# Kernel optimization log

Hardware: AMD Instinct MI355X
Metric: run time of the kernel (lower is better)

## Reference

```python
import jax, jax.numpy as jnp
import numpy as np

J = 25
C_IN, HID, LAT = 3, 64, 32


def _graph_conv(x, A, W, b):
    # x: [N,T,J,Cin]; A: [J,J]; W: [Cin,Cout]; b: [Cout]
    A = jax.nn.softmax(A, axis=-1)
    # fused adjacency mix + projection: (A @ x) @ W + b
    x = jnp.einsum('ij,ntjc->ntic', A, x)
    return jnp.einsum('ntjc,cd->ntjd', x, W) + b


def setup_inputs() -> dict:
    key = jax.random.key(0)
    ks = jax.random.split(key, 13)
    x = jax.random.normal(ks[0], (32, 2048, J, C_IN), dtype=jnp.float32)
    eye = jnp.eye(J, dtype=jnp.float32)
    def lin(kw, kb, cin, cout):
        W = jax.random.normal(kw, (cin, cout), dtype=jnp.float32) / np.sqrt(cin)
        b = jax.random.normal(kb, (cout,), dtype=jnp.float32) * 0.01
        return W, b
    W1, b1 = lin(ks[1], ks[2], C_IN, HID)
    W2, b2 = lin(ks[3], ks[4], HID, LAT)
    W3, b3 = lin(ks[5], ks[6], LAT, HID)
    W4, b4 = lin(ks[7], ks[8], HID, C_IN)
    return {
        'x': x,
        'A1': eye, 'W1': W1, 'b1': b1,
        'A2': eye, 'W2': W2, 'b2': b2,
        'A3': eye, 'W3': W3, 'b3': b3,
        'A4': eye, 'W4': W4, 'b4': b4,
    }


def reference(x, A1, W1, b1, A2, W2, b2, A3, W3, b3, A4, W4, b4):
    h = jax.nn.relu(_graph_conv(x, A1, W1, b1))     # encoder_g1 + relu
    z = _graph_conv(h, A2, W2, b2)                  # encoder_g2 (no relu)
    h_dec = jax.nn.relu(_graph_conv(z, A3, W3, b3)) # decoder_g1 + relu
    out = _graph_conv(h_dec, A4, W4, b4)            # decoder_g2
    return out
```

## Files before the change

kernel.cpp:

```cpp
#include <hip/hip_runtime.h>
#include <math.h>

#define J 25
#define NJC 75
#define NWAVE 4
#define NTHREADS 256
#define NFPW 8
#define FRSZ 1056
#define SCRW (2 * FRSZ)

#define O_A1T  0
#define O_APP  1024
#define O_A4B  2048
#define O_W2T  3072
#define O_W3T  5120
#define O_W1T  7168
#define O_W4C  8192
#define O_B4   8512
#define O_BPPF 8576
#define CWS_SZ 8704

using bf16x2 = __attribute__((ext_vector_type(2))) __bf16;
using bf16x8 = __attribute__((ext_vector_type(8))) __bf16;
using f32x4  = __attribute__((ext_vector_type(4))) float;
using f32x16 = __attribute__((ext_vector_type(16))) float;

__device__ inline bf16x8 zero8() {
    bf16x8 z;
    #pragma unroll
    for (int j = 0; j < 8; j++) z[j] = (__bf16)0.f;
    return z;
}

#if defined(__has_builtin)
#if __has_builtin(__builtin_amdgcn_cvt_pk_bf16_f32)
#define HAVE_PK_BF16 1
#endif
#endif

__device__ inline bf16x2 cvt2(float a, float b) {
#ifdef HAVE_PK_BF16
    return __builtin_amdgcn_cvt_pk_bf16_f32(a, b);
#else
    bf16x2 r; r[0] = (__bf16)a; r[1] = (__bf16)b; return r;
#endif
}
__device__ inline bf16x8 pk8(const f32x16& acc, int st) {
    const int b = 8 * st;
    bf16x8 r;
    #pragma unroll
    for (int p = 0; p < 4; p++) {
        bf16x2 v = cvt2(acc[b + 2 * p], acc[b + 2 * p + 1]);
        r[2 * p] = v[0]; r[2 * p + 1] = v[1];
    }
    return r;
}

__global__ __launch_bounds__(NTHREADS, 3) void gcn_fused(
    const float* __restrict__ x,
    const float* __restrict__ A1, const float* __restrict__ W1, const float* __restrict__ b1,
    const float* __restrict__ A2, const float* __restrict__ W2, const float* __restrict__ b2,
    const float* __restrict__ A3, const float* __restrict__ W3, const float* __restrict__ b3,
    const float* __restrict__ A4, const float* __restrict__ W4, const float* __restrict__ b4,
    float* __restrict__ out)
{
    __shared__ __align__(16) __bf16 SCR[NWAVE * SCRW];
    __shared__ __align__(16) __bf16 CWS[CWS_SZ];

    const int t = threadIdx.x;

    {
        float* T   = (float*)SCR;
        float* bpp = T + 3125;
        float* T0 = T;        float* T1 = T + 625;  float* T2 = T + 1250;
        float* T3 = T + 1875; float* T4 = T + 2500;

        if (t < 100) {
            const int m = t / J, i = t % J;
            const float* Asrc = (m == 0) ? A1 : (m == 1) ? A2 : (m == 2) ? A3 : A4;
            float row[J];
            float mx = -1e30f;
            #pragma unroll
            for (int j = 0; j < J; j++) { row[j] = Asrc[i * J + j]; mx = fmaxf(mx, row[j]); }
            float s = 0.f;
            #pragma unroll
            for (int j = 0; j < J; j++) { row[j] = __expf(row[j] - mx); s += row[j]; }
            const float inv = 1.f / s;
            float* dst = T + m * 625 + i * J;
            #pragma unroll
            for (int j = 0; j < J; j++) dst[j] = row[j] * inv;
        }
        if (t < 64) {
            float s = b3[t];
            #pragma unroll
            for (int l = 0; l < 32; l++) s += W3[l * 64 + t] * b2[l];
            bpp[t] = s;
        }
        __syncthreads();

        for (int idx = t; idx < 625; idx += 256) {
            const int i = idx / J, jj = idx % J;
            float s = 0.f;
            #pragma unroll
            for (int k = 0; k < J; k++) s += T2[i * J + k] * T1[k * J + jj];
            T4[idx] = s;
        }
        __syncthreads();

        for (int i = t; i < 1024; i += 256) {
            const int b = i >> 8, n = (i >> 3) & 31, jj = i & 7;
            const int kn = 8 * b + jj;
            CWS[O_A1T + i] = (__bf16)((kn < J && n < J) ? T0[n * J + kn] : 0.f);
            const int s = b >> 1, h = b & 1, r = 8 * s + jj;
            const int k32 = (r & 3) + 8 * (r >> 2) + 4 * h;
            CWS[O_APP + i] = (__bf16)((k32 < J && n < J) ? T4[n * J + k32] : 0.f);
            CWS[O_A4B + i] = (__bf16)((k32 < J && n < J) ? T3[n * J + k32] : 0.f);
        }
        for (int i = t; i < 2048; i += 256) {
            {
                const int b = i >> 8, n = (i >> 3) & 31, jj = i & 7;
                const int s = b >> 1, h = b & 1, r = 8 * (s & 1) + jj;
                const int d = 32 * (s >> 1) + (r & 3) + 8 * (r >> 2) + 4 * h;
                CWS[O_W2T + i] = (__bf16)W2[d * 32 + n];
            }
            {
                const int tt = i >> 10, rr = i & 1023;
                const int b = rr >> 8, m = (rr >> 3) & 31, jj = rr & 7;
                const int s = b >> 1, h = b & 1, r = 8 * s + jj;
                const int l = (r & 3) + 8 * (r >> 2) + 4 * h;
                CWS[O_W3T + i] = (__bf16)W3[l * 64 + tt * 32 + m];
            }
        }
        for (int i = t; i < 1024; i += 256) {
            const int tt = i >> 9, rq = i & 511, hf = rq >> 8, q = rq & 255;
            const int m = q >> 3, c = q & 7, d = tt * 32 + m;
            float v = 0.f;
            if (hf == 0) {
                if (c < 3) v = W1[c * 64 + d];
                else if (c == 3) v = b1[d];
            }
            CWS[O_W1T + i] = (__bf16)v;
        }
        {
            const int c = t >> 6, b = (t >> 3) & 7, jj = t & 7;
            const int s = b >> 1, h = b & 1, r = 8 * (s & 1) + jj;
            const int d = 32 * (s >> 1) + (r & 3) + 8 * (r >> 2) + 4 * h;
            CWS[O_W4C + t] = (c < 3) ? (__bf16)W4[d * 3 + c] : (__bf16)0.f;
        }
        {
            float* fwB = (float*)(CWS + O_BPPF);
            if (t < 64) {
                const int g = t >> 4, h = (t >> 3) & 1, jj = t & 7;
                const int tt = g >> 1, st = g & 1;
                const int row32 = (jj & 3) + 16 * st + 8 * (jj >> 2) + 4 * h;
                fwB[t] = bpp[tt * 32 + row32];
            }
            float* fb4 = (float*)(CWS + O_B4);
            if (t >= 64 && t < 68) fb4[t - 64] = (t < 67) ? b4[t - 64] : 0.f;
        }
        __syncthreads();
    }

    const int w = t >> 6, lane = t & 63, ln = lane & 31, half = lane >> 5;
    const int fo = ln * 8;
    __bf16* scr = &SCR[w * SCRW];

    const long fbase = ((long)blockIdx.x * NWAVE + w) * NFPW;

    #pragma unroll
    for (int r = 0; r < 2; r++) {
        __bf16* s = scr + r * FRSZ;
        if (half == 0) s[(ln >> 3) * 264 + 24 + (ln & 7)] = (ln < J) ? (__bf16)1.f : (__bf16)0.f;
        if (lane < 21) s[3 * 264 + (lane / 7) * 8 + 1 + (lane % 7)] = (__bf16)0.f;
    }

    const int c0 = lane % 3, j0 = lane / 3;
    const int sx0 = (j0 >> 3) * 264 + c0 * 8 + (j0 & 7);
    const int i1 = 64 + lane, c1 = i1 % 3, j1 = i1 / 3;
    const int sx1 = (j1 >> 3) * 264 + c1 * 8 + (j1 & 7);

    {
        const long xb = fbase * NJC;
        float v0 = x[xb + lane];
        float v1 = (lane < NJC - 64) ? x[xb + 64 + lane] : 0.f;
        scr[sx0] = (__bf16)v0;
        if (lane < NJC - 64) scr[sx1] = (__bf16)v1;
    }
    float xv0 = 0.f, xv1 = 0.f;
    if (NFPW > 1) {
        const long xb = (fbase + 1) * NJC;
        xv0 = x[xb + lane];
        if (lane < NJC - 64) xv1 = x[xb + 64 + lane];
    }

    bf16x8 rA1T[2], rApp[2], rA4b[2], rW1[2], rW4[4];
    #pragma unroll
    for (int ks = 0; ks < 2; ks++) {
        rA1T[ks] = *(const bf16x8*)&CWS[O_A1T + (2 * ks + half) * 256 + fo];
        rApp[ks] = *(const bf16x8*)&CWS[O_APP + (2 * ks + half) * 256 + fo];
        rA4b[ks] = *(const bf16x8*)&CWS[O_A4B + (2 * ks + half) * 256 + fo];
        rW1[ks]  = *(const bf16x8*)&CWS[O_W1T + ks * 512 + half * 256 + fo];
    }
    #pragma unroll
    for (int ks = 0; ks < 4; ks++) {
        rW4[ks] = zero8();
        if (ln < 3) rW4[ks] = *(const bf16x8*)&CWS[O_W4C + ln * 64 + (half + 2 * ks) * 8];
    }
    f32x16 rB16[2];
    {
        const float* fwB = (const float*)(CWS + O_BPPF);
        #pragma unroll
        for (int tt = 0; tt < 2; tt++)
            #pragma unroll
            for (int st = 0; st < 2; st++) {
                f32x4 qa = *(const f32x4*)&fwB[32 * tt + 16 * st + 8 * half + 0];
                f32x4 qb = *(const f32x4*)&fwB[32 * tt + 16 * st + 8 * half + 4];
                #pragma unroll
                for (int j = 0; j < 4; j++) {
                    rB16[tt][8 * st + j]     = qa[j];
                    rB16[tt][8 * st + 4 + j] = qb[j];
                }
            }
    }
    float b4v = 0.f;
    if (ln < 3) b4v = ((const float*)(CWS + O_B4))[ln];

    f32x16 Z;
    #pragma unroll
    for (int z = 0; z < 16; z++) Z[z] = 0.f;

    for (int fi = 0; fi < NFPW; fi++) {
        const long f = fbase + fi;
        __bf16* sc = scr + (fi & 1) * FRSZ;

        if (fi + 1 < NFPW) {
            __bf16* sn = scr + ((fi + 1) & 1) * FRSZ;
            sn[sx0] = (__bf16)xv0;
            if (lane < NJC - 64) sn[sx1] = (__bf16)xv1;
        }
        if (fi + 2 < NFPW) {
            const long nxb = (f + 2) * NJC;
            xv0 = x[nxb + lane];
            if (lane < NJC - 64) xv1 = x[nxb + 64 + lane];
        }

        bf16x8 a0 = *(const bf16x8*)&sc[half * 264 + fo];
        bf16x8 a1 = *(const bf16x8*)&sc[(2 + half) * 264 + fo];
        f32x16 accY = __builtin_amdgcn_mfma_f32_32x32x16_bf16(a0, rA1T[0], Z, 0, 0, 0);
        accY = __builtin_amdgcn_mfma_f32_32x32x16_bf16(a1, rA1T[1], accY, 0, 0, 0);

        bf16x8 w2f[4];
        #pragma unroll
        for (int s = 0; s < 4; s++)
            w2f[s] = *(const bf16x8*)&CWS[O_W2T + (half + 2 * s) * 256 + fo];

        bf16x8 yb = zero8();
        if (half == 0) {
            bf16x2 q0 = cvt2(accY[0], accY[1]);
            bf16x2 q1 = cvt2(accY[2], accY[3]);
            yb[0] = q0[0]; yb[1] = q0[1]; yb[2] = q1[0]; yb[3] = q1[1];
        }
        bf16x8 hf[4];
        #pragma unroll
        for (int tt = 0; tt < 2; tt++) {
            f32x16 acc = __builtin_amdgcn_mfma_f32_32x32x16_bf16(rW1[tt], yb, Z, 0, 0, 0);
            #pragma unroll
            for (int z = 0; z < 16; z++) acc[z] = fmaxf(acc[z], 0.f);
            hf[2 * tt]     = pk8(acc, 0);
            hf[2 * tt + 1] = pk8(acc, 1);
        }

        f32x16 accU = __builtin_amdgcn_mfma_f32_32x32x16_bf16(hf[0], w2f[0], Z, 0, 0, 0);
        #pragma unroll
        for (int s = 1; s < 4; s++)
            accU = __builtin_amdgcn_mfma_f32_32x32x16_bf16(hf[s], w2f[s], accU, 0, 0, 0);
        bf16x8 uf[2] = { pk8(accU, 0), pk8(accU, 1) };

        bf16x8 w3f[4];
        #pragma unroll
        for (int tt = 0; tt < 2; tt++)
            #pragma unroll
            for (int ks = 0; ks < 2; ks++)
                w3f[tt * 2 + ks] = *(const bf16x8*)&CWS[O_W3T + tt * 1024 + (half + 2 * ks) * 256 + fo];

        f32x16 accV = __builtin_amdgcn_mfma_f32_32x32x16_bf16(uf[0], rApp[0], Z, 0, 0, 0);
        accV = __builtin_amdgcn_mfma_f32_32x32x16_bf16(uf[1], rApp[1], accV, 0, 0, 0);
        bf16x8 vf[2] = { pk8(accV, 0), pk8(accV, 1) };

        bf16x8 hd[4];
        #pragma unroll
        for (int tt = 0; tt < 2; tt++) {
            f32x16 acc = __builtin_amdgcn_mfma_f32_32x32x16_bf16(w3f[tt * 2 + 0], vf[0], rB16[tt], 0, 0, 0);
            acc = __builtin_amdgcn_mfma_f32_32x32x16_bf16(w3f[tt * 2 + 1], vf[1], acc, 0, 0, 0);
            #pragma unroll
            for (int z = 0; z < 16; z++) acc[z] = fmaxf(acc[z], 0.f);
            hd[2 * tt]     = pk8(acc, 0);
            hd[2 * tt + 1] = pk8(acc, 1);
        }

        f32x16 accP = __builtin_amdgcn_mfma_f32_32x32x16_bf16(hd[0], rW4[0], Z, 0, 0, 0);
        #pragma unroll
        for (int s = 1; s < 4; s++)
            accP = __builtin_amdgcn_mfma_f32_32x32x16_bf16(hd[s], rW4[s], accP, 0, 0, 0);
        bf16x8 pf[2] = { pk8(accP, 0), pk8(accP, 1) };

        f32x16 accO = __builtin_amdgcn_mfma_f32_32x32x16_bf16(rA4b[0], pf[0], Z, 0, 0, 0);
        accO = __builtin_amdgcn_mfma_f32_32x32x16_bf16(rA4b[1], pf[1], accO, 0, 0, 0);
        if (ln < 3) {
            const long ob = f * NJC;
            #pragma unroll
            for (int r = 0; r < 16; r++) {
                const int row = (r & 3) + 8 * (r >> 2) + 4 * half;
                if (row < J) out[ob + row * 3 + ln] = accO[r] + b4v;
            }
        }
    }
}

extern "C" void kernel_launch(void* const* d_in, const int* in_sizes, int n_in,
                              void* d_out, int out_size, void* d_ws, size_t ws_size,
                              hipStream_t stream)
{
    const float* x  = (const float*)d_in[0];
    const float* A1 = (const float*)d_in[1];
    const float* W1 = (const float*)d_in[2];
    const float* b1 = (const float*)d_in[3];
    const float* A2 = (const float*)d_in[4];
    const float* W2 = (const float*)d_in[5];
    const float* b2 = (const float*)d_in[6];
    const float* A3 = (const float*)d_in[7];
    const float* W3 = (const float*)d_in[8];
    const float* b3 = (const float*)d_in[9];
    const float* A4 = (const float*)d_in[10];
    const float* W4 = (const float*)d_in[11];
    const float* b4 = (const float*)d_in[12];
    float* out = (float*)d_out;
    (void)d_ws; (void)ws_size;

    const int NT = in_sizes[0] / NJC;
    const int nblocks = NT / (NWAVE * NFPW);

    gcn_fused<<<nblocks, NTHREADS, 0, stream>>>(
        x, A1, W1, b1, A2, W2, b2, A3, W3, b3, A4, W4, b4, out);
}
```

Measured before the change: 147.5 us.

## Hoist W2/W3 fragments to registers, transpose final MFMA, double frames per wave

Loads the W2 and W3 weight fragments from shared memory into registers once, instead of reloading them on every frame. The final MFMA's operands are swapped so the output comes out transposed: each lane stores its joint's three channels directly, replacing 16 predicated scattered stores. Frames per wave go from 8 to 16, the frame loop is fully unrolled, and pointer arithmetic is made incremental. Occupancy is lowered to 2 blocks per CU to leave room for the extra registers, which costs latency hiding and halves the grid size.

```diff
diff --git a/kernel.cpp b/kernel.cpp
--- a/kernel.cpp
+++ b/kernel.cpp
@@ -5,7 +5,7 @@
 #define NJC 75
 #define NWAVE 4
 #define NTHREADS 256
-#define NFPW 8
+#define NFPW 16
 #define FRSZ 1056
 #define SCRW (2 * FRSZ)
 
@@ -56,7 +56,7 @@
     return r;
 }
 
-__global__ __launch_bounds__(NTHREADS, 3) void gcn_fused(
+__global__ __launch_bounds__(NTHREADS, 2) void gcn_fused(
     const float* __restrict__ x,
     const float* __restrict__ A1, const float* __restrict__ W1, const float* __restrict__ b1,
     const float* __restrict__ A2, const float* __restrict__ W2, const float* __restrict__ b2,
@@ -167,6 +167,9 @@
 
     const long fbase = ((long)blockIdx.x * NWAVE + w) * NFPW;
 
+    const float* xp = x + fbase * NJC;
+    float* op = out + fbase * NJC;
+
     #pragma unroll
     for (int r = 0; r < 2; r++) {
         __bf16* s = scr + r * FRSZ;
@@ -178,22 +181,21 @@
     const int sx0 = (j0 >> 3) * 264 + c0 * 8 + (j0 & 7);
     const int i1 = 64 + lane, c1 = i1 % 3, j1 = i1 / 3;
     const int sx1 = (j1 >> 3) * 264 + c1 * 8 + (j1 & 7);
+    const bool ld2 = (lane < NJC - 64);
 
     {
-        const long xb = fbase * NJC;
-        float v0 = x[xb + lane];
-        float v1 = (lane < NJC - 64) ? x[xb + 64 + lane] : 0.f;
-        scr[sx0] = (__bf16)v0;
-        if (lane < NJC - 64) scr[sx1] = (__bf16)v1;
+        scr[sx0] = (__bf16)xp[lane];
+        if (ld2) scr[sx1] = (__bf16)xp[64 + lane];
+        xp += NJC;
     }
     float xv0 = 0.f, xv1 = 0.f;
     if (NFPW > 1) {
-        const long xb = (fbase + 1) * NJC;
-        xv0 = x[xb + lane];
-        if (lane < NJC - 64) xv1 = x[xb + 64 + lane];
-    }
-
-    bf16x8 rA1T[2], rApp[2], rA4b[2], rW1[2], rW4[4];
+        xv0 = xp[lane];
+        if (ld2) xv1 = xp[64 + lane];
+        xp += NJC;
+    }
+
+    bf16x8 rA1T[2], rApp[2], rA4b[2], rW1[2], rW2[4], rW3[4], rW4[4];
     #pragma unroll
     for (int ks = 0; ks < 2; ks++) {
         rA1T[ks] = *(const bf16x8*)&CWS[O_A1T + (2 * ks + half) * 256 + fo];
@@ -201,6 +203,14 @@
         rA4b[ks] = *(const bf16x8*)&CWS[O_A4B + (2 * ks + half) * 256 + fo];
         rW1[ks]  = *(const bf16x8*)&CWS[O_W1T + ks * 512 + half * 256 + fo];
     }
+    #pragma unroll
+    for (int ks = 0; ks < 4; ks++)
+        rW2[ks] = *(const bf16x8*)&CWS[O_W2T + (half + 2 * ks) * 256 + fo];
+    #pragma unroll
+    for (int tt = 0; tt < 2; tt++)
+        #pragma unroll
+        for (int ks = 0; ks < 2; ks++)
+            rW3[tt * 2 + ks] = *(const bf16x8*)&CWS[O_W3T + tt * 1024 + (half + 2 * ks) * 256 + fo];
     #pragma unroll
     for (int ks = 0; ks < 4; ks++) {
         rW4[ks] = zero8();
@@ -222,37 +232,34 @@
                 }
             }
     }
-    float b4v = 0.f;
-    if (ln < 3) b4v = ((const float*)(CWS + O_B4))[ln];
+    const float* fb4 = (const float*)(CWS + O_B4);
+    const float b40 = fb4[0], b41 = fb4[1], b42 = fb4[2];
 
     f32x16 Z;
     #pragma unroll
     for (int z = 0; z < 16; z++) Z[z] = 0.f;
 
+    const bool do_store = (lane < J);
+
+    #pragma unroll
     for (int fi = 0; fi < NFPW; fi++) {
-        const long f = fbase + fi;
         __bf16* sc = scr + (fi & 1) * FRSZ;
 
         if (fi + 1 < NFPW) {
             __bf16* sn = scr + ((fi + 1) & 1) * FRSZ;
             sn[sx0] = (__bf16)xv0;
-            if (lane < NJC - 64) sn[sx1] = (__bf16)xv1;
+            if (ld2) sn[sx1] = (__bf16)xv1;
         }
         if (fi + 2 < NFPW) {
-            const long nxb = (f + 2) * NJC;
-            xv0 = x[nxb + lane];
-            if (lane < NJC - 64) xv1 = x[nxb + 64 + lane];
+            xv0 = xp[lane];
+            if (ld2) xv1 = xp[64 + lane];
+            xp += NJC;
         }
 
         bf16x8 a0 = *(const bf16x8*)&sc[half * 264 + fo];
         bf16x8 a1 = *(const bf16x8*)&sc[(2 + half) * 264 + fo];
         f32x16 accY = __builtin_amdgcn_mfma_f32_32x32x16_bf16(a0, rA1T[0], Z, 0, 0, 0);
         accY = __builtin_amdgcn_mfma_f32_32x32x16_bf16(a1, rA1T[1], accY, 0, 0, 0);
-
-        bf16x8 w2f[4];
-        #pragma unroll
-        for (int s = 0; s < 4; s++)
-            w2f[s] = *(const bf16x8*)&CWS[O_W2T + (half + 2 * s) * 256 + fo];
 
         bf16x8 yb = zero8();
         if (half == 0) {
@@ -270,18 +277,11 @@
             hf[2 * tt + 1] = pk8(acc, 1);
         }
 
-        f32x16 accU = __builtin_amdgcn_mfma_f32_32x32x16_bf16(hf[0], w2f[0], Z, 0, 0, 0);
+        f32x16 accU = __builtin_amdgcn_mfma_f32_32x32x16_bf16(hf[0], rW2[0], Z, 0, 0, 0);
         #pragma unroll
         for (int s = 1; s < 4; s++)
-            accU = __builtin_amdgcn_mfma_f32_32x32x16_bf16(hf[s], w2f[s], accU, 0, 0, 0);
+            accU = __builtin_amdgcn_mfma_f32_32x32x16_bf16(hf[s], rW2[s], accU, 0, 0, 0);
         bf16x8 uf[2] = { pk8(accU, 0), pk8(accU, 1) };
-
-        bf16x8 w3f[4];
-        #pragma unroll
-        for (int tt = 0; tt < 2; tt++)
-            #pragma unroll
-            for (int ks = 0; ks < 2; ks++)
-                w3f[tt * 2 + ks] = *(const bf16x8*)&CWS[O_W3T + tt * 1024 + (half + 2 * ks) * 256 + fo];
 
         f32x16 accV = __builtin_amdgcn_mfma_f32_32x32x16_bf16(uf[0], rApp[0], Z, 0, 0, 0);
         accV = __builtin_amdgcn_mfma_f32_32x32x16_bf16(uf[1], rApp[1], accV, 0, 0, 0);
@@ -290,8 +290,8 @@
         bf16x8 hd[4];
         #pragma unroll
         for (int tt = 0; tt < 2; tt++) {
-            f32x16 acc = __builtin_amdgcn_mfma_f32_32x32x16_bf16(w3f[tt * 2 + 0], vf[0], rB16[tt], 0, 0, 0);
-            acc = __builtin_amdgcn_mfma_f32_32x32x16_bf16(w3f[tt * 2 + 1], vf[1], acc, 0, 0, 0);
+            f32x16 acc = __builtin_amdgcn_mfma_f32_32x32x16_bf16(rW3[tt * 2 + 0], vf[0], rB16[tt], 0, 0, 0);
+            acc = __builtin_amdgcn_mfma_f32_32x32x16_bf16(rW3[tt * 2 + 1], vf[1], acc, 0, 0, 0);
             #pragma unroll
             for (int z = 0; z < 16; z++) acc[z] = fmaxf(acc[z], 0.f);
             hd[2 * tt]     = pk8(acc, 0);
@@ -304,16 +304,14 @@
             accP = __builtin_amdgcn_mfma_f32_32x32x16_bf16(hd[s], rW4[s], accP, 0, 0, 0);
         bf16x8 pf[2] = { pk8(accP, 0), pk8(accP, 1) };
 
-        f32x16 accO = __builtin_amdgcn_mfma_f32_32x32x16_bf16(rA4b[0], pf[0], Z, 0, 0, 0);
-        accO = __builtin_amdgcn_mfma_f32_32x32x16_bf16(rA4b[1], pf[1], accO, 0, 0, 0);
-        if (ln < 3) {
-            const long ob = f * NJC;
-            #pragma unroll
-            for (int r = 0; r < 16; r++) {
-                const int row = (r & 3) + 8 * (r >> 2) + 4 * half;
-                if (row < J) out[ob + row * 3 + ln] = accO[r] + b4v;
-            }
-        }
+        f32x16 accO = __builtin_amdgcn_mfma_f32_32x32x16_bf16(pf[0], rA4b[0], Z, 0, 0, 0);
+        accO = __builtin_amdgcn_mfma_f32_32x32x16_bf16(pf[1], rA4b[1], accO, 0, 0, 0);
+        if (do_store) {
+            op[lane * 3 + 0] = accO[0] + b40;
+            op[lane * 3 + 1] = accO[1] + b41;
+            op[lane * 3 + 2] = accO[2] + b42;
+        }
+        op += NJC;
     }
 }
 
```

Result: faster. 140.0 us (-5.1%).
